# Kernel tuning notes

Measured on AMD Instinct MI355X. Metric: run time of the kernel, lower is better.

Reference implementation:

```python
import jax, jax.numpy as jnp
import numpy as np

TAU = 0.8
LAM = 0.5
N1 = N2 = 4096
H = 512
DENSITY = 0.004


def _build_indices():
    rng = np.random.default_rng(4)
    md = (rng.random((N1, N2)) < DENSITY)
    ones = np.argwhere(md)          # [P, 2] positive (i, j) pairs
    zeros = np.argwhere(~md)        # negative pairs
    rng.shuffle(ones)
    sel = rng.permutation(len(zeros))[: len(ones)]
    zeros = zeros[sel]
    return (ones[:, 0].astype(np.int32), ones[:, 1].astype(np.int32),
            zeros[:, 0].astype(np.int32), zeros[:, 1].astype(np.int32))


def setup_inputs() -> dict:
    key = jax.random.key(0)
    ks = jax.random.split(key, 10)
    z_mp1 = jax.random.normal(ks[0], (N1, H), jnp.float32)
    z_sc1 = jax.random.normal(ks[1], (N1, H), jnp.float32)
    z_mp2 = jax.random.normal(ks[2], (N2, H), jnp.float32)
    z_sc2 = jax.random.normal(ks[3], (N2, H), jnp.float32)
    # positive masks: identity plus a few random extra positives (pos.to_dense())
    pos1 = (jnp.eye(N1, dtype=jnp.float32)
            + (jax.random.uniform(ks[4], (N1, N1)) < 0.001).astype(jnp.float32))
    pos1 = jnp.minimum(pos1, 1.0)
    pos2 = (jnp.eye(N2, dtype=jnp.float32)
            + (jax.random.uniform(ks[5], (N2, N2)) < 0.001).astype(jnp.float32))
    pos2 = jnp.minimum(pos2, 1.0)
    # proj params (xavier-normal-ish scale)
    s = (2.0 / (H + H)) ** 0.5 * 1.414
    W1 = jax.random.normal(ks[6], (H, H), jnp.float32) * s
    b1 = jnp.zeros((H,), jnp.float32)
    W2 = jax.random.normal(ks[7], (H, H), jnp.float32) * s
    b2 = jnp.zeros((H,), jnp.float32)
    pi, pj, ni, nj = _build_indices()
    return dict(z_mp1=z_mp1, z_sc1=z_sc1, pos1=pos1,
                z_mp2=z_mp2, z_sc2=z_sc2, pos2=pos2,
                W1=W1, b1=b1, W2=W2, b2=b2,
                pos_i=jnp.asarray(pi), pos_j=jnp.asarray(pj),
                neg_i=jnp.asarray(ni), neg_j=jnp.asarray(nj))


def _proj(z, W1, b1, W2, b2):
    h = jax.nn.elu(z @ W1.T + b1)
    return h @ W2.T + b2


def _sim(z1, z2):
    num = z1 @ z2.T
    den = (jnp.linalg.norm(z1, axis=-1, keepdims=True)
           @ jnp.linalg.norm(z2, axis=-1, keepdims=True).T)
    return jnp.exp(num / den / TAU)


def _gclloss(z_mp, z_sc, pos, W1, b1, W2, b2):
    zm = _proj(z_mp, W1, b1, W2, b2)
    zs = _proj(z_sc, W1, b1, W2, b2)
    m = _sim(zm, zs)                 # [N, N]
    mt = m.T
    m = m / (m.sum(axis=1, keepdims=True) + 1e-8)
    lori_mp = -jnp.log((m * pos).sum(axis=-1)).mean()
    mt = mt / (mt.sum(axis=1, keepdims=True) + 1e-8)
    lori_sc = -jnp.log((mt * pos).sum(axis=-1)).mean()
    return LAM * lori_mp + (1.0 - LAM) * lori_sc


def reference(z_mp1, z_sc1, pos1, z_mp2, z_sc2, pos2,
              W1, b1, W2, b2, pos_i, pos_j, neg_i, neg_j):
    # vectorized replacement of the per-sample torch.dot loops
    pm = z_mp1[pos_i] + z_sc1[pos_i]
    pd = z_mp2[pos_j] + z_sc2[pos_j]
    ip1 = (pm * pd).sum(-1)
    nm = z_mp1[neg_i] + z_sc1[neg_i]
    nd = z_mp2[neg_j] + z_sc2[neg_j]
    ip2 = (nm * nd).sum(-1)
    # original wraps scalars in torch.tensor(...), detaching them from the graph
    ip1 = jax.lax.stop_gradient(ip1)
    ip2 = jax.lax.stop_gradient(ip2)
    loss_main = (-jnp.mean(jax.nn.log_sigmoid(ip1))
                 + jnp.mean(jax.nn.log_sigmoid(-ip2)))
    loss1 = _gclloss(z_mp1, z_sc1, pos1, W1, b1, W2, b2)
    loss2 = _gclloss(z_mp2, z_sc2, pos2, W1, b1, W2, b2)
    return loss_main + loss1 + loss2
```

## Files before the change

### kernel.cpp

```cpp
#include <hip/hip_runtime.h>
#include <math.h>

#define TAU_INV 1.25f
#define LAMBDA 0.5f
#define NR 4096
#define HD 512

typedef __attribute__((ext_vector_type(8))) short short8;
typedef __attribute__((ext_vector_type(4))) float f32x4;
typedef __attribute__((ext_vector_type(4))) unsigned short ushort4v;

static __device__ __forceinline__ unsigned short f2bf(float f) {
  unsigned int u = __float_as_uint(f);
  u += 0x7fff + ((u >> 16) & 1);
  return (unsigned short)(u >> 16);
}
static __device__ __forceinline__ float bf2f(unsigned short s) {
  return __uint_as_float(((unsigned int)s) << 16);
}

__global__ __launch_bounds__(256) void cast_bf16(const float* __restrict__ src,
                                                 unsigned short* __restrict__ dst, int n4) {
  int i = blockIdx.x * 256 + threadIdx.x;
  if (i < n4) {
    float4 v = ((const float4*)src)[i];
    ushort4v o;
    o.x = f2bf(v.x); o.y = f2bf(v.y); o.z = f2bf(v.z); o.w = f2bf(v.w);
    ((ushort4v*)dst)[i] = o;
  }
}

__global__ __launch_bounds__(256) void addz(const float* __restrict__ a,
                                            const float* __restrict__ b,
                                            float* __restrict__ o, int n4) {
  int i = blockIdx.x * 256 + threadIdx.x;
  if (i < n4) {
    float4 x = ((const float4*)a)[i], y = ((const float4*)b)[i];
    float4 r; r.x = x.x + y.x; r.y = x.y + y.y; r.z = x.z + y.z; r.w = x.w + y.w;
    ((float4*)o)[i] = r;
  }
}


#define GEMM_STAGE(Aptr, Bptr, rb, cb_, kb)                                                     \
  {                                                                                             \
    _Pragma("unroll") for (int q = 0; q < 4; ++q) {                                             \
      int r0 = q * 32 + w * 8;                                                                  \
      const char* sa = (const char*)(Aptr) + ((size_t)((rb) + r0 + lrow) << 10) + (kb)*128 + scb;\
      const char* sb = (const char*)(Bptr) + ((size_t)((cb_) + r0 + lrow) << 10) + (kb)*128 + scb;\
      __builtin_amdgcn_global_load_lds((const __attribute__((address_space(1))) unsigned int*)sa,\
          (__attribute__((address_space(3))) unsigned int*)(void*)((char*)As + r0 * 128), 16, 0, 0);\
      __builtin_amdgcn_global_load_lds((const __attribute__((address_space(1))) unsigned int*)sb,\
          (__attribute__((address_space(3))) unsigned int*)(void*)((char*)Bs + r0 * 128), 16, 0, 0);\
    }                                                                                           \
  }

#define GEMM_COMPUTE()                                                                          \
  {                                                                                             \
    _Pragma("unroll") for (int kk = 0; kk < 2; ++kk) {                                          \
      short8 av[4], bv[4];                                                                      \
      _Pragma("unroll") for (int mf = 0; mf < 4; ++mf) {                                        \
        int row = wr * 64 + mf * 16 + (l & 15);                                                 \
        int kbyte = ((kk * 64) + ((l >> 4) * 16)) ^ ((l & 7) << 4);                             \
        av[mf] = *(const short8*)((const char*)As + row * 128 + kbyte);                         \
      }                                                                                        \
      _Pragma("unroll") for (int nf = 0; nf < 4; ++nf) {                                        \
        int row = wc * 64 + nf * 16 + (l & 15);                                                 \
        int kbyte = ((kk * 64) + ((l >> 4) * 16)) ^ ((l & 7) << 4);                             \
        bv[nf] = *(const short8*)((const char*)Bs + row * 128 + kbyte);                         \
      }                                                                                        \
      _Pragma("unroll") for (int mf = 0; mf < 4; ++mf)                                          \
        _Pragma("unroll") for (int nf = 0; nf < 4; ++nf)                                        \
          acc[mf][nf] = __builtin_amdgcn_mfma_f32_16x16x32_bf16(av[mf], bv[nf], acc[mf][nf], 0, 0, 0);\
    }                                                                                           \
  }

template <bool DO_ELU>
__global__ __launch_bounds__(256) void proj_mfma(const unsigned short* __restrict__ A0,
                                                 const unsigned short* __restrict__ A1,
                                                 const unsigned short* __restrict__ B,
                                                 const float* __restrict__ bias,
                                                 unsigned short* __restrict__ C0,
                                                 unsigned short* __restrict__ C1) {
  __shared__ unsigned short As[128 * 64];
  __shared__ unsigned short Bs[128 * 64];
  const int tid = threadIdx.x;
  const int l = tid & 63, w = tid >> 6;
  const int wr = w >> 1, wc = w & 1;
  const int stream_id = blockIdx.y >> 5;
  const int rowbase = (blockIdx.y & 31) * 128;
  const int colbase = blockIdx.x * 128;
  const unsigned short* A = stream_id ? A1 : A0;
  unsigned short* C = stream_id ? C1 : C0;
  const int lrow = l >> 3;
  const int scb = ((l & 7) ^ lrow) << 4;

  f32x4 acc[4][4];
#pragma unroll
  for (int i = 0; i < 4; ++i)
#pragma unroll
    for (int j = 0; j < 4; ++j) acc[i][j] = (f32x4){0.f, 0.f, 0.f, 0.f};

  for (int kb = 0; kb < 8; ++kb) {
    GEMM_STAGE(A, B, rowbase, colbase, kb);
    __syncthreads();
    GEMM_COMPUTE();
    __syncthreads();
  }

  const int cq = l >> 4, cn = l & 15;
#pragma unroll
  for (int mf = 0; mf < 4; ++mf) {
#pragma unroll
    for (int nf = 0; nf < 4; ++nf) {
      int col = colbase + wc * 64 + nf * 16 + cn;
      float bb = bias[col];
#pragma unroll
      for (int j = 0; j < 4; ++j) {
        int row = rowbase + wr * 64 + mf * 16 + cq * 4 + j;
        float v = acc[mf][nf][j] + bb;
        if (DO_ELU) v = v > 0.f ? v : expm1f(v);
        C[(size_t)row * HD + col] = f2bf(v);
      }
    }
  }
}

__global__ __launch_bounds__(256) void rownorm_bf(const unsigned short* __restrict__ Z,
                                                  float* __restrict__ inv, int rows) {
  int wid = blockIdx.x * 4 + (threadIdx.x >> 6);
  int lane = threadIdx.x & 63;
  if (wid >= rows) return;
  short8 v = ((const short8*)(Z + (size_t)wid * HD))[lane];
  float s = 0.f;
#pragma unroll
  for (int j = 0; j < 8; ++j) {
    float f = bf2f((unsigned short)v[j]);
    s += f * f;
  }
#pragma unroll
  for (int off = 1; off < 64; off <<= 1) s += __shfl_xor(s, off);
  if (lane == 0) inv[wid] = 1.f / sqrtf(s);
}

__global__ __launch_bounds__(256) void sim_mfma(const unsigned short* __restrict__ PA,
                                                const unsigned short* __restrict__ PB,
                                                const float* __restrict__ invA,
                                                const float* __restrict__ invB,
                                                const float* __restrict__ pos,
                                                float* __restrict__ accRS,
                                                float* __restrict__ accRP,
                                                float* __restrict__ accCS,
                                                float* __restrict__ accCP) {
  __shared__ unsigned short As[128 * 64];
  __shared__ unsigned short Bs[128 * 64];
  const int tid = threadIdx.x;
  const int l = tid & 63, w = tid >> 6;
  const int wr = w >> 1, wc = w & 1;
  const int rowbase = blockIdx.y * 128;
  const int colbase = blockIdx.x * 128;
  const int lrow = l >> 3;
  const int scb = ((l & 7) ^ lrow) << 4;

  f32x4 acc[4][4];
#pragma unroll
  for (int i = 0; i < 4; ++i)
#pragma unroll
    for (int j = 0; j < 4; ++j) acc[i][j] = (f32x4){0.f, 0.f, 0.f, 0.f};

  for (int kb = 0; kb < 8; ++kb) {
    GEMM_STAGE(PA, PB, rowbase, colbase, kb);
    __syncthreads();
    GEMM_COMPUTE();
    __syncthreads();
  }

  const int cq = l >> 4, cn = l & 15;
  float sr[4][4], sc[4];
#pragma unroll
  for (int mf = 0; mf < 4; ++mf) {
    float4 iv = *(const float4*)(invA + rowbase + wr * 64 + mf * 16 + cq * 4);
    sr[mf][0] = iv.x * TAU_INV; sr[mf][1] = iv.y * TAU_INV;
    sr[mf][2] = iv.z * TAU_INV; sr[mf][3] = iv.w * TAU_INV;
  }
#pragma unroll
  for (int nf = 0; nf < 4; ++nf) sc[nf] = invB[colbase + wc * 64 + nf * 16 + cn];

#pragma unroll
  for (int mf = 0; mf < 4; ++mf)
#pragma unroll
    for (int nf = 0; nf < 4; ++nf)
#pragma unroll
      for (int j = 0; j < 4; ++j)
        acc[mf][nf][j] = expf(acc[mf][nf][j] * sr[mf][j] * sc[nf]);

#pragma unroll
  for (int mf = 0; mf < 4; ++mf) {
    float rs[4] = {0.f, 0.f, 0.f, 0.f}, rp[4] = {0.f, 0.f, 0.f, 0.f};
#pragma unroll
    for (int nf = 0; nf < 4; ++nf) {
      int col = colbase + wc * 64 + nf * 16 + cn;
#pragma unroll
      for (int j = 0; j < 4; ++j) {
        float m = acc[mf][nf][j];
        rs[j] += m;
        float p = pos[(size_t)(rowbase + wr * 64 + mf * 16 + cq * 4 + j) * NR + col];
        rp[j] += m * p;
      }
    }
#pragma unroll
    for (int off = 1; off < 16; off <<= 1) {
#pragma unroll
      for (int j = 0; j < 4; ++j) { rs[j] += __shfl_xor(rs[j], off); rp[j] += __shfl_xor(rp[j], off); }
    }
    if (cn == 0) {
#pragma unroll
      for (int j = 0; j < 4; ++j) {
        int row = rowbase + wr * 64 + mf * 16 + cq * 4 + j;
        atomicAdd(&accRS[row], rs[j]);
        atomicAdd(&accRP[row], rp[j]);
      }
    }
  }

  float cs[4] = {0.f, 0.f, 0.f, 0.f}, cp[4] = {0.f, 0.f, 0.f, 0.f};
#pragma unroll
  for (int nf = 0; nf < 4; ++nf) {
    int col = colbase + wc * 64 + nf * 16 + cn;
#pragma unroll
    for (int mf = 0; mf < 4; ++mf) {
      float4 pT = *(const float4*)(pos + (size_t)col * NR + rowbase + wr * 64 + mf * 16 + cq * 4);
      float pj[4] = {pT.x, pT.y, pT.z, pT.w};
#pragma unroll
      for (int j = 0; j < 4; ++j) { cs[nf] += acc[mf][nf][j]; cp[nf] += acc[mf][nf][j] * pj[j]; }
    }
  }
#pragma unroll
  for (int off = 16; off < 64; off <<= 1) {
#pragma unroll
    for (int nf = 0; nf < 4; ++nf) { cs[nf] += __shfl_xor(cs[nf], off); cp[nf] += __shfl_xor(cp[nf], off); }
  }
  if (cq == 0) {
#pragma unroll
    for (int nf = 0; nf < 4; ++nf) {
      int col = colbase + wc * 64 + nf * 16 + cn;
      atomicAdd(&accCS[col], cs[nf]);
      atomicAdd(&accCP[col], cp[nf]);
    }
  }
}

__global__ __launch_bounds__(256) void pair_logsig(const float* __restrict__ ZS1,
                                                   const float* __restrict__ ZS2,
                                                   const int* __restrict__ pi,
                                                   const int* __restrict__ pj,
                                                   const int* __restrict__ ni,
                                                   const int* __restrict__ nj,
                                                   int P, float* __restrict__ lsig) {
  int wid = blockIdx.x * 4 + (threadIdx.x >> 6);
  int lane = threadIdx.x & 63;
  if (wid >= 2 * P) return;
  bool isneg = wid >= P;
  int p = isneg ? wid - P : wid;
  int i = isneg ? ni[p] : pi[p];
  int j = isneg ? nj[p] : pj[p];
  const float4* a = (const float4*)(ZS1 + (size_t)i * HD);
  const float4* b = (const float4*)(ZS2 + (size_t)j * HD);
  float s = 0.f;
#pragma unroll
  for (int t = 0; t < 2; ++t) {
    float4 x = a[lane * 2 + t], y = b[lane * 2 + t];
    s += x.x * y.x + x.y * y.y + x.z * y.z + x.w * y.w;
  }
#pragma unroll
  for (int off = 1; off < 64; off <<= 1) s += __shfl_xor(s, off);
  if (lane == 0) {
    float ip = isneg ? -s : s;
    lsig[wid] = fminf(ip, 0.f) - log1pf(expf(-fabsf(ip)));
  }
}

#define RED_BLOCKS 128
__global__ __launch_bounds__(256) void reduce_partial(const float* __restrict__ acc,
                                                      const float* __restrict__ lsig,
                                                      int P, float* __restrict__ part) {
  __shared__ float red[6][4];
  int tid = threadIdx.x;
  int gid = blockIdx.x * 256 + tid;
  int stride = gridDim.x * 256;
  float loc[6] = {0.f, 0.f, 0.f, 0.f, 0.f, 0.f};
  for (int idx = gid; idx < 2 * NR; idx += stride) {
    int l = idx >> 12, i = idx & (NR - 1);
    const float* base = acc + (size_t)l * 4 * NR;
    float t0 = logf(base[NR + i] / (base[i] + 1e-8f));
    float t1 = logf(base[3 * NR + i] / (base[2 * NR + i] + 1e-8f));
    if (l == 0) { loc[0] += t0; loc[1] += t1; }
    else        { loc[2] += t0; loc[3] += t1; }
  }
  for (int i = gid; i < P; i += stride) loc[4] += lsig[i];
  for (int i = gid; i < P; i += stride) loc[5] += lsig[P + i];
  int wv = tid >> 6, ln = tid & 63;
#pragma unroll
  for (int q = 0; q < 6; ++q) {
    float s = loc[q];
#pragma unroll
    for (int off = 1; off < 64; off <<= 1) s += __shfl_xor(s, off);
    if (ln == 0) red[q][wv] = s;
  }
  __syncthreads();
  if (tid < 6) part[blockIdx.x * 6 + tid] = red[tid][0] + red[tid][1] + red[tid][2] + red[tid][3];
}

__global__ __launch_bounds__(64) void finalize2(const float* __restrict__ part,
                                                int P, float* __restrict__ out) {
  int ln = threadIdx.x;
  float t[6];
#pragma unroll
  for (int q = 0; q < 6; ++q) {
    float s = part[ln * 6 + q] + part[(ln + 64) * 6 + q];
#pragma unroll
    for (int off = 1; off < 64; off <<= 1) s += __shfl_xor(s, off);
    t[q] = s;
  }
  if (ln == 0) {
    float loss1 = LAMBDA * (-t[0] / (float)NR) + (1.f - LAMBDA) * (-t[1] / (float)NR);
    float loss2 = LAMBDA * (-t[2] / (float)NR) + (1.f - LAMBDA) * (-t[3] / (float)NR);
    float loss_main = -(t[4] / (float)P) + (t[5] / (float)P);
    out[0] = loss_main + loss1 + loss2;
  }
}

extern "C" void kernel_launch(void* const* d_in, const int* in_sizes, int n_in,
                              void* d_out, int out_size, void* d_ws, size_t ws_size,
                              hipStream_t stream) {
  const float* z_mp1 = (const float*)d_in[0];
  const float* z_sc1 = (const float*)d_in[1];
  const float* pos1 = (const float*)d_in[2];
  const float* z_mp2 = (const float*)d_in[3];
  const float* z_sc2 = (const float*)d_in[4];
  const float* pos2 = (const float*)d_in[5];
  const float* W1 = (const float*)d_in[6];
  const float* b1 = (const float*)d_in[7];
  const float* W2 = (const float*)d_in[8];
  const float* b2 = (const float*)d_in[9];
  const int* pi = (const int*)d_in[10];
  const int* pj = (const int*)d_in[11];
  const int* ni = (const int*)d_in[12];
  const int* nj = (const int*)d_in[13];
  const int P = in_sizes[10];

  char* ws = (char*)d_ws;
  float* ACC = (float*)(ws);
  float* PART = ACC + 8 * 4096;
  float* INV = (float*)(ws + 256 * 1024);
  float* LSIG = (float*)(ws + 320 * 1024);
  unsigned short* ZB0 = (unsigned short*)(ws + 2 * 1024 * 1024);
  unsigned short* ZB1 = (unsigned short*)(ws + 6 * 1024 * 1024);
  unsigned short* W1b = (unsigned short*)(ws + 10 * 1024 * 1024);
  unsigned short* W2b = (unsigned short*)(ws + 10 * 1024 * 1024 + 512 * 1024);
  float* ZSUM1 = (float*)(ws + 12 * 1024 * 1024);
  float* ZSUM2 = (float*)(ws + 20 * 1024 * 1024);
  unsigned short* HBm = (unsigned short*)(ws + 12 * 1024 * 1024);
  unsigned short* HBs = (unsigned short*)(ws + 16 * 1024 * 1024);
  unsigned short* PAb = (unsigned short*)(ws + 20 * 1024 * 1024);
  unsigned short* PBb = (unsigned short*)(ws + 24 * 1024 * 1024);

  hipMemsetAsync(ACC, 0, 16 * 4096 * sizeof(float), stream);

  cast_bf16<<<256, 256, 0, stream>>>(W1, W1b, 512 * 512 / 4);
  cast_bf16<<<256, 256, 0, stream>>>(W2, W2b, 512 * 512 / 4);
  addz<<<2048, 256, 0, stream>>>(z_mp1, z_sc1, ZSUM1, NR * HD / 4);
  addz<<<2048, 256, 0, stream>>>(z_mp2, z_sc2, ZSUM2, NR * HD / 4);
  pair_logsig<<<(2 * P + 3) / 4, 256, 0, stream>>>(ZSUM1, ZSUM2, pi, pj, ni, nj, P, LSIG);

  dim3 gP(4, 64);
  dim3 gS(32, 32);
  for (int ll = 0; ll < 2; ++ll) {
    const float* zm = ll ? z_mp2 : z_mp1;
    const float* zs = ll ? z_sc2 : z_sc1;
    const float* pos = ll ? pos2 : pos1;
    cast_bf16<<<2048, 256, 0, stream>>>(zm, ZB0, NR * HD / 4);
    cast_bf16<<<2048, 256, 0, stream>>>(zs, ZB1, NR * HD / 4);
    proj_mfma<true><<<gP, 256, 0, stream>>>(ZB0, ZB1, W1b, b1, HBm, HBs);
    proj_mfma<false><<<gP, 256, 0, stream>>>(HBm, HBs, W2b, b2, PAb, PBb);
    rownorm_bf<<<1024, 256, 0, stream>>>(PAb, INV, NR);
    rownorm_bf<<<1024, 256, 0, stream>>>(PBb, INV + 4096, NR);
    sim_mfma<<<gS, 256, 0, stream>>>(PAb, PBb, INV, INV + 4096, pos,
                                     ACC + (size_t)(ll * 4 + 0) * 4096, ACC + (size_t)(ll * 4 + 1) * 4096,
                                     ACC + (size_t)(ll * 4 + 2) * 4096, ACC + (size_t)(ll * 4 + 3) * 4096);
  }
  reduce_partial<<<RED_BLOCKS, 256, 0, stream>>>(ACC, LSIG, P, PART);
  finalize2<<<1, 64, 0, stream>>>(PART, P, (float*)d_out);
}
```

Measured before the change: 418.2 us.

## Pack positive masks into bitmasks and store z-sums in bf16

Adds a pre-pass that compresses each dense fp32 positive mask into a bit-per-entry bitmap using wave ballots. The similarity kernel then reads mask bits instead of fp32 values for both row and column sums, which removes the strided transposed fp32 pos reads. The z_mp+z_sc sums are also written as bf16, halving the gather traffic in the pair dot-product kernel at some cost in precision. The pack pass still reads each full 64MB mask once, and the workspace layout is rearranged.

```diff
diff --git a/kernel.cpp b/kernel.cpp
--- a/kernel.cpp
+++ b/kernel.cpp
@@ -30,14 +30,29 @@
   }
 }
 
-__global__ __launch_bounds__(256) void addz(const float* __restrict__ a,
-                                            const float* __restrict__ b,
-                                            float* __restrict__ o, int n4) {
+__global__ __launch_bounds__(256) void addz_bf(const float* __restrict__ a,
+                                               const float* __restrict__ b,
+                                               unsigned short* __restrict__ o, int n4) {
   int i = blockIdx.x * 256 + threadIdx.x;
   if (i < n4) {
     float4 x = ((const float4*)a)[i], y = ((const float4*)b)[i];
-    float4 r; r.x = x.x + y.x; r.y = x.y + y.y; r.z = x.z + y.z; r.w = x.w + y.w;
-    ((float4*)o)[i] = r;
+    ushort4v r;
+    r.x = f2bf(x.x + y.x); r.y = f2bf(x.y + y.y);
+    r.z = f2bf(x.z + y.z); r.w = f2bf(x.w + y.w);
+    ((ushort4v*)o)[i] = r;
+  }
+}
+
+__global__ __launch_bounds__(256) void pos_pack(const float* __restrict__ pos,
+                                                unsigned long long* __restrict__ bits) {
+  int lane = threadIdx.x & 63;
+  int gw = (blockIdx.x * 256 + threadIdx.x) >> 6;
+  int stride = (gridDim.x * 256) >> 6;
+  const int nwords = NR * NR / 64;
+  for (int w = gw; w < nwords; w += stride) {
+    float v = pos[(size_t)w * 64 + lane];
+    unsigned long long m = __ballot(v > 0.5f);
+    if (lane == 0) bits[w] = m;
   }
 }
 
@@ -147,7 +162,7 @@
                                                 const unsigned short* __restrict__ PB,
                                                 const float* __restrict__ invA,
                                                 const float* __restrict__ invB,
-                                                const float* __restrict__ pos,
+                                                const unsigned int* __restrict__ BM,
                                                 float* __restrict__ accRS,
                                                 float* __restrict__ accRP,
                                                 float* __restrict__ accCS,
@@ -198,14 +213,16 @@
   for (int mf = 0; mf < 4; ++mf) {
     float rs[4] = {0.f, 0.f, 0.f, 0.f}, rp[4] = {0.f, 0.f, 0.f, 0.f};
 #pragma unroll
-    for (int nf = 0; nf < 4; ++nf) {
-      int col = colbase + wc * 64 + nf * 16 + cn;
-#pragma unroll
-      for (int j = 0; j < 4; ++j) {
+    for (int j = 0; j < 4; ++j) {
+      int row = rowbase + wr * 64 + mf * 16 + cq * 4 + j;
+      const unsigned int* bmr = BM + (size_t)row * 128 + (colbase >> 5) + wc * 2;
+      unsigned int w0 = bmr[0], w1 = bmr[1];
+#pragma unroll
+      for (int nf = 0; nf < 4; ++nf) {
         float m = acc[mf][nf][j];
         rs[j] += m;
-        float p = pos[(size_t)(rowbase + wr * 64 + mf * 16 + cq * 4 + j) * NR + col];
-        rp[j] += m * p;
+        unsigned int wsel = (nf < 2) ? w0 : w1;
+        if ((wsel >> ((nf * 16 + cn) & 31)) & 1) rp[j] += m;
       }
     }
 #pragma unroll
@@ -227,12 +244,17 @@
 #pragma unroll
   for (int nf = 0; nf < 4; ++nf) {
     int col = colbase + wc * 64 + nf * 16 + cn;
+    const unsigned int* bmc = BM + (size_t)col * 128 + (rowbase >> 5) + wr * 2;
+    unsigned int w0 = bmc[0], w1 = bmc[1];
 #pragma unroll
     for (int mf = 0; mf < 4; ++mf) {
-      float4 pT = *(const float4*)(pos + (size_t)col * NR + rowbase + wr * 64 + mf * 16 + cq * 4);
-      float pj[4] = {pT.x, pT.y, pT.z, pT.w};
-#pragma unroll
-      for (int j = 0; j < 4; ++j) { cs[nf] += acc[mf][nf][j]; cp[nf] += acc[mf][nf][j] * pj[j]; }
+      unsigned int wsel = (mf < 2) ? w0 : w1;
+#pragma unroll
+      for (int j = 0; j < 4; ++j) {
+        float m = acc[mf][nf][j];
+        cs[nf] += m;
+        if ((wsel >> ((mf * 16 + cq * 4 + j) & 31)) & 1) cp[nf] += m;
+      }
     }
   }
 #pragma unroll
@@ -250,8 +272,8 @@
   }
 }
 
-__global__ __launch_bounds__(256) void pair_logsig(const float* __restrict__ ZS1,
-                                                   const float* __restrict__ ZS2,
+__global__ __launch_bounds__(256) void pair_logsig(const unsigned short* __restrict__ ZS1,
+                                                   const unsigned short* __restrict__ ZS2,
                                                    const int* __restrict__ pi,
                                                    const int* __restrict__ pj,
                                                    const int* __restrict__ ni,
@@ -264,14 +286,12 @@
   int p = isneg ? wid - P : wid;
   int i = isneg ? ni[p] : pi[p];
   int j = isneg ? nj[p] : pj[p];
-  const float4* a = (const float4*)(ZS1 + (size_t)i * HD);
-  const float4* b = (const float4*)(ZS2 + (size_t)j * HD);
+  short8 a = ((const short8*)(ZS1 + (size_t)i * HD))[lane];
+  short8 b = ((const short8*)(ZS2 + (size_t)j * HD))[lane];
   float s = 0.f;
 #pragma unroll
-  for (int t = 0; t < 2; ++t) {
-    float4 x = a[lane * 2 + t], y = b[lane * 2 + t];
-    s += x.x * y.x + x.y * y.y + x.z * y.z + x.w * y.w;
-  }
+  for (int t = 0; t < 8; ++t)
+    s = fmaf(bf2f((unsigned short)a[t]), bf2f((unsigned short)b[t]), s);
 #pragma unroll
   for (int off = 1; off < 64; off <<= 1) s += __shfl_xor(s, off);
   if (lane == 0) {
@@ -352,40 +372,44 @@
   char* ws = (char*)d_ws;
   float* ACC = (float*)(ws);
   float* PART = ACC + 8 * 4096;
-  float* INV = (float*)(ws + 256 * 1024);
-  float* LSIG = (float*)(ws + 320 * 1024);
+  float* INV = (float*)(ws + 260 * 1024);
+  float* LSIG = (float*)(ws + 300 * 1024);
+  unsigned short* W1b = (unsigned short*)(ws + 1024 * 1024);
+  unsigned short* W2b = (unsigned short*)(ws + 1536 * 1024);
   unsigned short* ZB0 = (unsigned short*)(ws + 2 * 1024 * 1024);
   unsigned short* ZB1 = (unsigned short*)(ws + 6 * 1024 * 1024);
-  unsigned short* W1b = (unsigned short*)(ws + 10 * 1024 * 1024);
-  unsigned short* W2b = (unsigned short*)(ws + 10 * 1024 * 1024 + 512 * 1024);
-  float* ZSUM1 = (float*)(ws + 12 * 1024 * 1024);
-  float* ZSUM2 = (float*)(ws + 20 * 1024 * 1024);
-  unsigned short* HBm = (unsigned short*)(ws + 12 * 1024 * 1024);
-  unsigned short* HBs = (unsigned short*)(ws + 16 * 1024 * 1024);
-  unsigned short* PAb = (unsigned short*)(ws + 20 * 1024 * 1024);
-  unsigned short* PBb = (unsigned short*)(ws + 24 * 1024 * 1024);
+  unsigned short* ZSB1 = (unsigned short*)(ws + 10 * 1024 * 1024);
+  unsigned short* ZSB2 = (unsigned short*)(ws + 14 * 1024 * 1024);
+  unsigned short* HBm = (unsigned short*)(ws + 10 * 1024 * 1024);
+  unsigned short* HBs = (unsigned short*)(ws + 14 * 1024 * 1024);
+  unsigned short* PAb = (unsigned short*)(ws + 18 * 1024 * 1024);
+  unsigned short* PBb = (unsigned short*)(ws + 22 * 1024 * 1024);
+  unsigned long long* PU1 = (unsigned long long*)(ws + 26 * 1024 * 1024);
+  unsigned long long* PU2 = (unsigned long long*)(ws + 28 * 1024 * 1024);
 
   hipMemsetAsync(ACC, 0, 16 * 4096 * sizeof(float), stream);
 
   cast_bf16<<<256, 256, 0, stream>>>(W1, W1b, 512 * 512 / 4);
   cast_bf16<<<256, 256, 0, stream>>>(W2, W2b, 512 * 512 / 4);
-  addz<<<2048, 256, 0, stream>>>(z_mp1, z_sc1, ZSUM1, NR * HD / 4);
-  addz<<<2048, 256, 0, stream>>>(z_mp2, z_sc2, ZSUM2, NR * HD / 4);
-  pair_logsig<<<(2 * P + 3) / 4, 256, 0, stream>>>(ZSUM1, ZSUM2, pi, pj, ni, nj, P, LSIG);
+  addz_bf<<<2048, 256, 0, stream>>>(z_mp1, z_sc1, ZSB1, NR * HD / 4);
+  addz_bf<<<2048, 256, 0, stream>>>(z_mp2, z_sc2, ZSB2, NR * HD / 4);
+  pair_logsig<<<(2 * P + 3) / 4, 256, 0, stream>>>(ZSB1, ZSB2, pi, pj, ni, nj, P, LSIG);
+  pos_pack<<<2048, 256, 0, stream>>>(pos1, PU1);
+  pos_pack<<<2048, 256, 0, stream>>>(pos2, PU2);
 
   dim3 gP(4, 64);
   dim3 gS(32, 32);
   for (int ll = 0; ll < 2; ++ll) {
     const float* zm = ll ? z_mp2 : z_mp1;
     const float* zs = ll ? z_sc2 : z_sc1;
-    const float* pos = ll ? pos2 : pos1;
+    const unsigned int* bm = (const unsigned int*)(ll ? PU2 : PU1);
     cast_bf16<<<2048, 256, 0, stream>>>(zm, ZB0, NR * HD / 4);
     cast_bf16<<<2048, 256, 0, stream>>>(zs, ZB1, NR * HD / 4);
     proj_mfma<true><<<gP, 256, 0, stream>>>(ZB0, ZB1, W1b, b1, HBm, HBs);
     proj_mfma<false><<<gP, 256, 0, stream>>>(HBm, HBs, W2b, b2, PAb, PBb);
     rownorm_bf<<<1024, 256, 0, stream>>>(PAb, INV, NR);
     rownorm_bf<<<1024, 256, 0, stream>>>(PBb, INV + 4096, NR);
-    sim_mfma<<<gS, 256, 0, stream>>>(PAb, PBb, INV, INV + 4096, pos,
+    sim_mfma<<<gS, 256, 0, stream>>>(PAb, PBb, INV, INV + 4096, bm,
                                      ACC + (size_t)(ll * 4 + 0) * 4096, ACC + (size_t)(ll * 4 + 1) * 4096,
                                      ACC + (size_t)(ll * 4 + 2) * 4096, ACC + (size_t)(ll * 4 + 3) * 4096);
   }
```

Measured after the change: 431.7 us. 1.03x slower.
